# Performance work log

Hardware: AMD Instinct MI355X
Metric: run time of the kernel (lower is better)

Reference implementation:

```python
import jax, jax.numpy as jnp
import numpy as np

BN_EPS = 1e-5
ALPHA = 0.3
NEG = -9e9
BN_SCALE = 1.0 / np.sqrt(1.0 + BN_EPS)  # eval BatchNorm with running_mean=0, running_var=1


def gat_layer(x, mask, W, a, bn_g, bn_b, concat):
    # x: [B,N,Fin], mask: [B,N,N] bool, W: [Fin,Fo], a: [2*Fo]
    h = jnp.einsum('bnf,fo->bno', x, W)               # [B,N,Fo]
    Fo = W.shape[1]
    s1 = h @ a[:Fo]                                    # [B,N]
    s2 = h @ a[Fo:]                                    # [B,N]
    # additive decomposition of concat([h_i, h_j]) @ a (identical math)
    e = jax.nn.leaky_relu(s1[:, :, None] + s2[:, None, :], ALPHA)  # [B,N,N]
    att = jax.nn.softmax(jnp.where(mask, e, NEG), axis=-1)
    hp = jnp.einsum('bnm,bmo->bno', att, h)            # [B,N,Fo]
    # BatchNorm1d(nodes_num) in eval mode, per-node-channel affine
    hp = hp * BN_SCALE * bn_g[None, :, None] + bn_b[None, :, None]
    return jax.nn.elu(hp) if concat else hp


def setup_inputs() -> dict:
    key = jax.random.key(0)
    ks = jax.random.split(key, 10)
    B, N, F, Fo, H, C = 128, 200, 768, 32, 8, 2
    Fh = Fo * H
    return {
        'feat_matrix': jax.random.normal(ks[0], (B, N, F), jnp.float32),
        'adj': jax.random.randint(ks[1], (B, N, N), 0, 2, jnp.int32),
        'W_heads': jax.random.normal(ks[2], (H, F, Fo), jnp.float32) * 0.05,
        'a_heads': jax.random.normal(ks[3], (H, 2 * Fo), jnp.float32) * 0.1,
        'bnh_g': jnp.ones((H, N), jnp.float32),
        'bnh_b': jnp.zeros((H, N), jnp.float32),
        'bnt_g': jnp.ones((N,), jnp.float32),
        'bnt_b': jnp.zeros((N,), jnp.float32),
        'W_sent': jax.random.normal(ks[4], (Fh, C), jnp.float32) * 0.1,
        'a_sent': jax.random.normal(ks[5], (2 * C,), jnp.float32) * 0.1,
        'bns_g': jnp.ones((N,), jnp.float32),
        'bns_b': jnp.zeros((N,), jnp.float32),
        'W_para': jax.random.normal(ks[6], (Fh, C), jnp.float32) * 0.1,
        'a_para': jax.random.normal(ks[7], (2 * C,), jnp.float32) * 0.1,
        'bnp_g': jnp.ones((N,), jnp.float32),
        'bnp_b': jnp.zeros((N,), jnp.float32),
        'W_q': jax.random.normal(ks[8], (Fh, Fo), jnp.float32) * 0.1,
        'a_q': jax.random.normal(ks[9], (2 * Fo,), jnp.float32) * 0.1,
        'bnq_g': jnp.ones((N,), jnp.float32),
        'bnq_b': jnp.zeros((N,), jnp.float32),
        'W2': jax.random.normal(jax.random.fold_in(key, 99), (Fo, 2), jnp.float32) * 0.1,
    }


def reference(feat_matrix, adj, W_heads, a_heads, bnh_g, bnh_b, bnt_g, bnt_b,
              W_sent, a_sent, bns_g, bns_b, W_para, a_para, bnp_g, bnp_b,
              W_q, a_q, bnq_g, bnq_b, W2):
    mask = adj > 0
    # 8 attention heads (concat=True), vmapped over head dim
    heads = jax.vmap(lambda W, a, g, b: gat_layer(feat_matrix, mask, W, a, g, b, True))(
        W_heads, a_heads, bnh_g, bnh_b)              # [H,B,N,Fo]
    H, B, N, Fo = heads.shape
    x = jnp.moveaxis(heads, 0, 2).reshape(B, N, H * Fo)  # head-major concat, matches torch.cat
    # top-level BatchNorm1d (eval) + dropout(no-op)
    x = x * BN_SCALE * bnt_g[None, :, None] + bnt_b[None, :, None]
    logits_sent = jax.nn.sigmoid(gat_layer(x, mask, W_sent, a_sent, bns_g, bns_b, False))
    logits_para = jax.nn.elu(gat_layer(x, mask, W_para, a_para, bnp_g, bnp_b, False))
    q = gat_layer(x, mask, W_q, a_q, bnq_g, bnq_b, False)[:, 0, :]   # [B,Fo]
    logits_Qtype = jax.nn.elu(q @ W2).reshape(-1, 2)
    return (logits_sent, logits_para, logits_Qtype)
```

## Files before the change

kernel.cpp:

```cpp
#include <hip/hip_runtime.h>
#include <hip/hip_bf16.h>
#include <cstdint>

#define BN_SCALEF 0.99999500003749975f
#define EXP_SHIFT 4.0f


typedef _Float16 half8 __attribute__((ext_vector_type(8)));
typedef _Float16 half4 __attribute__((ext_vector_type(4)));
typedef float floatx4 __attribute__((ext_vector_type(4)));


__global__ __launch_bounds__(256) void prep(const int* __restrict__ adj,
                                            const float* __restrict__ W_heads,
                                            const float* __restrict__ Ws_in,
                                            const float* __restrict__ Wp_in,
                                            const float* __restrict__ Wq_in,
                                            const float* __restrict__ a_sent,
                                            const float* __restrict__ a_para,
                                            const float* __restrict__ a_q,
                                            unsigned int* __restrict__ maskw,
                                            _Float16* __restrict__ Bt,
                                            _Float16* __restrict__ W2t48) {
    int blk = blockIdx.x;
    int t = threadIdx.x;
    if (blk < 1600) {
        int w = t >> 6, lane = t & 63;
        for (int task = w; task < 64; task += 4) {
            int r = blk * 16 + (task >> 2);
            int c0 = (task & 3) * 64;
            int j = c0 + lane;
            bool v = (j < 200) && (adj[(size_t)r * 200 + j] > 0);
            unsigned long long m = __ballot(v ? 1 : 0);
            if (lane == 0) {
                maskw[r * 8 + (c0 >> 5)]     = (unsigned int)(m & 0xffffffffULL);
                maskw[r * 8 + (c0 >> 5) + 1] = (unsigned int)(m >> 32);
            }
        }
    } else if (blk < 1792) {
        __shared__ float ld[32][36];
        int blk2 = blk - 1600;
        int h = blk2 / 24, f0 = (blk2 % 24) * 32;
        int idx = t * 4;
        int fr = idx >> 5, o0 = idx & 31;
        float4 v = *(const float4*)&W_heads[(size_t)h * 24576 + (size_t)(f0 + fr) * 32 + o0];
        ld[fr][o0] = v.x; ld[fr][o0 + 1] = v.y; ld[fr][o0 + 2] = v.z; ld[fr][o0 + 3] = v.w;
        __syncthreads();
        int o = idx >> 5, fr0 = idx & 31;
        half4 hv;
#pragma unroll
        for (int u = 0; u < 4; ++u) hv[u] = (_Float16)ld[fr0 + u][o];
        *(half4*)&Bt[(size_t)(h * 32 + o) * 768 + f0 + fr0] = hv;
    } else {
        int k = t;
        for (int c = 0; c < 36; ++c) {
            float v;
            if (c < 2)      v = Ws_in[k * 2 + c];
            else if (c < 4) v = Wp_in[k * 2 + (c - 2)];
            else            v = Wq_in[k * 32 + (c - 4)];
            W2t48[c * 256 + k] = (_Float16)v;
        }
        W2t48[36 * 256 + k] = (_Float16)(Ws_in[k * 2] * a_sent[0] + Ws_in[k * 2 + 1] * a_sent[1]);
        W2t48[37 * 256 + k] = (_Float16)(Ws_in[k * 2] * a_sent[2] + Ws_in[k * 2 + 1] * a_sent[3]);
        W2t48[38 * 256 + k] = (_Float16)(Wp_in[k * 2] * a_para[0] + Wp_in[k * 2 + 1] * a_para[1]);
        W2t48[39 * 256 + k] = (_Float16)(Wp_in[k * 2] * a_para[2] + Wp_in[k * 2 + 1] * a_para[3]);
        float q1 = 0.f, q2 = 0.f;
#pragma unroll
        for (int o = 0; o < 32; ++o) {
            q1 += Wq_in[k * 32 + o] * a_q[o];
            q2 += Wq_in[k * 32 + o] * a_q[32 + o];
        }
        W2t48[40 * 256 + k] = (_Float16)q1;
        W2t48[41 * 256 + k] = (_Float16)q2;
        for (int c = 42; c < 48; ++c) W2t48[c * 256 + k] = (_Float16)0.f;
    }
}


__global__ __launch_bounds__(256) void gemm1_mfma(const float* __restrict__ A,
                                                  const _Float16* __restrict__ Bt,
                                                  _Float16* __restrict__ h16) {
    __shared__ __align__(16) _Float16 As[32 * 776];
    int t = threadIdx.x;
    int m0 = blockIdx.x * 32;

    {
        int row = t >> 3, kb = (t & 7) * 4;
        const float* ap = &A[(size_t)(m0 + row) * 768 + kb];
        _Float16* lp = &As[row * 776 + kb];
#pragma unroll
        for (int j = 0; j < 24; ++j) {
            float4 v = *(const float4*)(ap + j * 32);
            half4 hv;
            hv[0] = (_Float16)v.x; hv[1] = (_Float16)v.y;
            hv[2] = (_Float16)v.z; hv[3] = (_Float16)v.w;
            *(half4*)(lp + j * 32) = hv;
        }
    }
    __syncthreads();

    int w = t >> 6, lane = t & 63;
    int l16 = lane & 15, quad = lane >> 4;
    int c0 = w * 64;

    floatx4 acc[2][4];
#pragma unroll
    for (int i = 0; i < 2; ++i)
#pragma unroll
        for (int j = 0; j < 4; ++j) acc[i][j] = (floatx4){0.f, 0.f, 0.f, 0.f};

    const _Float16* bbase = &Bt[(size_t)(c0 + l16) * 768 + quad * 8];

    half8 nb[4];
#pragma unroll
    for (int ct = 0; ct < 4; ++ct)
        nb[ct] = *(const half8*)(bbase + (size_t)ct * 12288);

#pragma unroll 4
    for (int k0 = 0; k0 < 768; k0 += 32) {
        half8 bf0 = nb[0], bf1 = nb[1], bf2 = nb[2], bf3 = nb[3];
        int kn = (k0 + 32 < 768) ? (k0 + 32) : 0;
#pragma unroll
        for (int ct = 0; ct < 4; ++ct)
            nb[ct] = *(const half8*)(bbase + (size_t)ct * 12288 + kn);

        half8 af0 = *(half8*)&As[l16 * 776 + k0 + quad * 8];
        half8 af1 = *(half8*)&As[(16 + l16) * 776 + k0 + quad * 8];

        acc[0][0] = __builtin_amdgcn_mfma_f32_16x16x32_f16(af0, bf0, acc[0][0], 0, 0, 0);
        acc[1][0] = __builtin_amdgcn_mfma_f32_16x16x32_f16(af1, bf0, acc[1][0], 0, 0, 0);
        acc[0][1] = __builtin_amdgcn_mfma_f32_16x16x32_f16(af0, bf1, acc[0][1], 0, 0, 0);
        acc[1][1] = __builtin_amdgcn_mfma_f32_16x16x32_f16(af1, bf1, acc[1][1], 0, 0, 0);
        acc[0][2] = __builtin_amdgcn_mfma_f32_16x16x32_f16(af0, bf2, acc[0][2], 0, 0, 0);
        acc[1][2] = __builtin_amdgcn_mfma_f32_16x16x32_f16(af1, bf2, acc[1][2], 0, 0, 0);
        acc[0][3] = __builtin_amdgcn_mfma_f32_16x16x32_f16(af0, bf3, acc[0][3], 0, 0, 0);
        acc[1][3] = __builtin_amdgcn_mfma_f32_16x16x32_f16(af1, bf3, acc[1][3], 0, 0, 0);
    }

#pragma unroll
    for (int rt = 0; rt < 2; ++rt)
#pragma unroll
        for (int ct = 0; ct < 4; ++ct) {
            int gc = c0 + ct * 16 + l16;
#pragma unroll
            for (int r = 0; r < 4; ++r) {
                int gr = m0 + rt * 16 + quad * 4 + r;
                h16[(size_t)gr * 256 + gc] = (_Float16)acc[rt][ct][r];
            }
        }
}


__global__ __launch_bounds__(256) void attn_heads_mfma(
    const _Float16* __restrict__ h16,
    const float* __restrict__ a_h,
    const unsigned int* __restrict__ maskw,
    const float* __restrict__ bnh_g, const float* __restrict__ bnh_b,
    const float* __restrict__ bnt_g, const float* __restrict__ bnt_b,
    _Float16* __restrict__ x16h) {
    __shared__ __align__(16) _Float16 Bs[48 * 228];
    __shared__ __align__(16) _Float16 Ps[64 * 228];
    __shared__ float s1s[256], s2s[256];
    int hb = blockIdx.x;
    int h = hb >> 7, b = hb & 127;
    int t = threadIdx.x;

    unsigned long long* bz = (unsigned long long*)Bs;
    for (int idx = t; idx < (48 * 228) / 4; idx += 256) bz[idx] = 0ULL;
    __syncthreads();
    for (int idx = t; idx < 800; idx += 256) {
        int j = idx >> 2, w8 = (idx & 3) * 8;
        half8 v = *(const half8*)&h16[(size_t)(b * 200 + j) * 256 + h * 32 + w8];
#pragma unroll
        for (int u = 0; u < 8; ++u) Bs[(w8 + u) * 228 + j] = v[u];
    }
    if (t < 200) Bs[32 * 228 + t] = (_Float16)1.0f;
    __syncthreads();

    if (t < 200) {
        float acc1 = 0.f, acc2 = 0.f;
        const float* ab = &a_h[h * 64];
#pragma unroll
        for (int o = 0; o < 32; ++o) {
            float hv = (float)Bs[o * 228 + t];
            acc1 += hv * ab[o];
            acc2 += hv * ab[32 + o];
        }
        s1s[t] = acc1; s2s[t] = acc2;
    } else {
        s1s[t] = 0.f; s2s[t] = 0.f;
    }
    __syncthreads();

    int w = t >> 6, lane = t & 63;
    int l16 = lane & 15, quad = lane >> 4;
    _Float16* Pw = &Ps[w * 16 * 228];

    int j0 = lane * 4;
    float4 s2r = *(const float4*)&s2s[j0];
    const unsigned int* mbase = &maskw[(size_t)(b * 200) * 8 + (lane >> 3)];

    for (int tile = w; tile < 13; tile += 4) {
        int i_base = tile * 16;
        unsigned int mw = mbase[(size_t)i_base * 8];
        for (int r16 = 0; r16 < 16; ++r16) {
            int i = i_base + r16;
            unsigned int mw_next = 0;
            if (r16 < 15) {
                int in = i + 1; in = in < 200 ? in : 199;
                mw_next = mbase[(size_t)in * 8];
            }
            float s1v = s1s[i];
            half4 pv;
#pragma unroll
            for (int q = 0; q < 4; ++q) {
                float e = s1v + ((const float*)&s2r)[q];
                e = fmaxf(e, 0.3f * e);
                float p = ((mw >> ((j0 + q) & 31)) & 1u) ? __expf(e - EXP_SHIFT) : 0.f;
                pv[q] = (_Float16)p;
            }
            if (j0 < 228) *(half4*)&Pw[r16 * 228 + j0] = pv;
            mw = mw_next;
        }
        floatx4 acc0 = {0.f, 0.f, 0.f, 0.f};
        floatx4 acc1 = {0.f, 0.f, 0.f, 0.f};
        floatx4 acc2 = {0.f, 0.f, 0.f, 0.f};
#pragma unroll
        for (int kt = 0; kt < 7; ++kt) {
            half8 af = *(half8*)&Pw[l16 * 228 + kt * 32 + quad * 8];
            half8 b0 = *(half8*)&Bs[(l16) * 228 + kt * 32 + quad * 8];
            half8 b1 = *(half8*)&Bs[(16 + l16) * 228 + kt * 32 + quad * 8];
            half8 b2 = *(half8*)&Bs[(32 + l16) * 228 + kt * 32 + quad * 8];
            acc0 = __builtin_amdgcn_mfma_f32_16x16x32_f16(af, b0, acc0, 0, 0, 0);
            acc1 = __builtin_amdgcn_mfma_f32_16x16x32_f16(af, b1, acc1, 0, 0, 0);
            acc2 = __builtin_amdgcn_mfma_f32_16x16x32_f16(af, b2, acc2, 0, 0, 0);
        }
#pragma unroll
        for (int r = 0; r < 4; ++r) {
            int i = i_base + quad * 4 + r;
            float rsum = __shfl(acc2[r], (lane & 48), 64);
            if (i < 200) {
                float inv = 1.f / rsum;
                float g1 = BN_SCALEF * bnh_g[h * 200 + i], c1 = bnh_b[h * 200 + i];
                float g2 = BN_SCALEF * bnt_g[i], c2 = bnt_b[i];
                float v0 = acc0[r] * inv * g1 + c1;
                v0 = v0 > 0.f ? v0 : __expf(v0) - 1.f;
                v0 = v0 * g2 + c2;
                float v1 = acc1[r] * inv * g1 + c1;
                v1 = v1 > 0.f ? v1 : __expf(v1) - 1.f;
                v1 = v1 * g2 + c2;
                size_t base = (size_t)h * 819200 + (size_t)(b * 200 + i) * 32;
                x16h[base + l16]      = (_Float16)v0;
                x16h[base + 16 + l16] = (_Float16)v1;
            }
        }
    }
}


__global__ __launch_bounds__(256) void gemm2m(const _Float16* __restrict__ Xh,
                                              const _Float16* __restrict__ Wt,
                                              float* __restrict__ H2p) {
    __shared__ __align__(16) _Float16 Xs[64 * 264];
    __shared__ __align__(16) _Float16 Ws[48 * 264];
    int t = threadIdx.x;
    int m0 = blockIdx.x * 64;
    int srow = t >> 2, schunk = (t & 3) * 8;
#pragma unroll
    for (int h = 0; h < 8; ++h) {
        half8 v = *(const half8*)&Xh[(size_t)h * 819200 + (size_t)(m0 + srow) * 32 + schunk];
        *(half8*)&Xs[srow * 264 + h * 32 + schunk] = v;
    }
#pragma unroll
    for (int p = 0; p < 6; ++p) {
        int g = t + 256 * p;
        int n = g >> 5, ko = (g & 31) * 8;
        *(half8*)&Ws[n * 264 + ko] = *(const half8*)&Wt[(size_t)n * 256 + ko];
    }
    __syncthreads();

    int w = t >> 6, lane = t & 63;
    int l16 = lane & 15, quad = lane >> 4;
    int rbase = w * 16;
    floatx4 acc[3];
#pragma unroll
    for (int c = 0; c < 3; ++c) acc[c] = (floatx4){0.f, 0.f, 0.f, 0.f};
#pragma unroll
    for (int kt = 0; kt < 8; ++kt) {
        half8 af = *(half8*)&Xs[(rbase + l16) * 264 + kt * 32 + quad * 8];
#pragma unroll
        for (int ct = 0; ct < 3; ++ct) {
            half8 bf = *(half8*)&Ws[(ct * 16 + l16) * 264 + kt * 32 + quad * 8];
            acc[ct] = __builtin_amdgcn_mfma_f32_16x16x32_f16(af, bf, acc[ct], 0, 0, 0);
        }
    }
#pragma unroll
    for (int ct = 0; ct < 3; ++ct) {
        int col = ct * 16 + l16;
#pragma unroll
        for (int r = 0; r < 4; ++r) {
            int row = m0 + rbase + quad * 4 + r;
            H2p[(size_t)row * 48 + col] = acc[ct][r];
        }
    }
}


__global__ __launch_bounds__(256) void attn_spq(const float* __restrict__ H2p,
                                                const unsigned int* __restrict__ maskw,
                                                const float* __restrict__ bns_g, const float* __restrict__ bns_b,
                                                const float* __restrict__ bnp_g, const float* __restrict__ bnp_b,
                                                const float* __restrict__ bnq_g, const float* __restrict__ bnq_b,
                                                const float* __restrict__ W2, float* __restrict__ out) {
    int b = blockIdx.x;
    int t = threadIdx.x;
    if (blockIdx.y == 2) {
        __shared__ float p_lds[200];
        __shared__ float redd[4];
        __shared__ float red2[256];
        float s1v = H2p[(size_t)(b * 200) * 48 + 40];
        float p = 0.f;
        if (t < 200) {
            unsigned int mw = maskw[(size_t)(b * 200) * 8 + (t >> 5)];
            if ((mw >> (t & 31)) & 1u) {
                float x = s1v + H2p[(size_t)(b * 200 + t) * 48 + 41];
                x = fmaxf(x, 0.3f * x);
                p = __expf(x - EXP_SHIFT);
            }
            p_lds[t] = p;
        }
        float ds = p;
        for (int off = 32; off; off >>= 1) ds += __shfl_xor(ds, off, 64);
        if ((t & 63) == 0) redd[t >> 6] = ds;
        __syncthreads();
        ds = redd[0] + redd[1] + redd[2] + redd[3];
        int o = t & 31, g = t >> 5;
        float acc = 0.f;
        for (int j = g; j < 200; j += 8)
            acc += p_lds[j] * H2p[(size_t)(b * 200 + j) * 48 + 4 + o];
        red2[t] = acc;
        __syncthreads();
        if (t < 32) {
            float s = 0.f;
#pragma unroll
            for (int gg = 0; gg < 8; ++gg) s += red2[gg * 32 + t];
            float qv = (s / ds) * (BN_SCALEF * bnq_g[0]) + bnq_b[0];
            float c0 = qv * W2[t * 2], c1 = qv * W2[t * 2 + 1];
#pragma unroll
            for (int off = 16; off; off >>= 1) {
                c0 += __shfl_xor(c0, off, 64);
                c1 += __shfl_xor(c1, off, 64);
            }
            if (t == 0) {
                out[102400 + b * 2 + 0] = c0 > 0.f ? c0 : __expf(c0) - 1.f;
                out[102400 + b * 2 + 1] = c1 > 0.f ? c1 : __expf(c1) - 1.f;
            }
        }
        return;
    }
    __shared__ float s2s[200], s2p[200];
    __shared__ float s1sA[200], s1pA[200];
    __shared__ __align__(16) float hsp[200 * 4];
    int chunk = blockIdx.y;
    if (t < 200) {
        const float* hr = &H2p[(size_t)(b * 200 + t) * 48];
        float4 hv = *(const float4*)hr;
        *(float4*)&hsp[t * 4] = hv;
        s1sA[t] = hr[36]; s2s[t] = hr[37];
        s1pA[t] = hr[38]; s2p[t] = hr[39];
    }
    __syncthreads();
    int w = t >> 6, lane = t & 63;
    for (int it = 0; it < 25; ++it) {
        int i = chunk * 100 + it * 4 + w;
        float s1sv = s1sA[i];
        float s1pv = s1pA[i];
        float ds = 0.f, dp = 0.f, pa0 = 0.f, pa1 = 0.f, pb0 = 0.f, pb1 = 0.f;
#pragma unroll
        for (int q = 0; q < 4; ++q) {
            int j = lane + 64 * q;
            if (j < 200) {
                unsigned int mw = maskw[(size_t)(b * 200 + i) * 8 + (j >> 5)];
                if ((mw >> (j & 31)) & 1u) {
                    float x1 = s1sv + s2s[j]; x1 = fmaxf(x1, 0.3f * x1);
                    float x2 = s1pv + s2p[j]; x2 = fmaxf(x2, 0.3f * x2);
                    float p1 = __expf(x1 - EXP_SHIFT), p2 = __expf(x2 - EXP_SHIFT);
                    ds += p1; dp += p2;
                    float4 hv = *(float4*)&hsp[j * 4];
                    pa0 += p1 * hv.x; pa1 += p1 * hv.y;
                    pb0 += p2 * hv.z; pb1 += p2 * hv.w;
                }
            }
        }
        for (int off = 32; off; off >>= 1) {
            ds  += __shfl_xor(ds, off, 64);  dp  += __shfl_xor(dp, off, 64);
            pa0 += __shfl_xor(pa0, off, 64); pa1 += __shfl_xor(pa1, off, 64);
            pb0 += __shfl_xor(pb0, off, 64); pb1 += __shfl_xor(pb1, off, 64);
        }
        if (lane == 0) {
            float gs = BN_SCALEF * bns_g[i], bs = bns_b[i];
            float v0 = (pa0 / ds) * gs + bs, v1 = (pa1 / ds) * gs + bs;
            out[(size_t)(b * 200 + i) * 2 + 0] = 1.f / (1.f + __expf(-v0));
            out[(size_t)(b * 200 + i) * 2 + 1] = 1.f / (1.f + __expf(-v1));
            float gp = BN_SCALEF * bnp_g[i], bp = bnp_b[i];
            float u0 = (pb0 / dp) * gp + bp, u1 = (pb1 / dp) * gp + bp;
            out[51200 + (size_t)(b * 200 + i) * 2 + 0] = u0 > 0.f ? u0 : __expf(u0) - 1.f;
            out[51200 + (size_t)(b * 200 + i) * 2 + 1] = u1 > 0.f ? u1 : __expf(u1) - 1.f;
        }
    }
}


extern "C" void kernel_launch(void* const* d_in, const int* in_sizes, int n_in,
                              void* d_out, int out_size, void* d_ws, size_t ws_size,
                              hipStream_t stream) {
    (void)in_sizes; (void)n_in; (void)out_size; (void)ws_size;
    const float* feat    = (const float*)d_in[0];
    const int*   adj     = (const int*)d_in[1];
    const float* W_heads = (const float*)d_in[2];
    const float* a_heads = (const float*)d_in[3];
    const float* bnh_g   = (const float*)d_in[4];
    const float* bnh_b   = (const float*)d_in[5];
    const float* bnt_g   = (const float*)d_in[6];
    const float* bnt_b   = (const float*)d_in[7];
    const float* W_sent  = (const float*)d_in[8];
    const float* a_sent  = (const float*)d_in[9];
    const float* bns_g   = (const float*)d_in[10];
    const float* bns_b   = (const float*)d_in[11];
    const float* W_para  = (const float*)d_in[12];
    const float* a_para  = (const float*)d_in[13];
    const float* bnp_g   = (const float*)d_in[14];
    const float* bnp_b   = (const float*)d_in[15];
    const float* W_q     = (const float*)d_in[16];
    const float* a_q     = (const float*)d_in[17];
    const float* bnq_g   = (const float*)d_in[18];
    const float* bnq_b   = (const float*)d_in[19];
    const float* W2      = (const float*)d_in[20];
    float* out = (float*)d_out;
    float* ws  = (float*)d_ws;

    _Float16* h16   = (_Float16*)ws;
    _Float16* x16h  = (_Float16*)(ws + 3276800);
    _Float16* W2t48 = (_Float16*)(ws + 6553600);
    _Float16* Bt    = (_Float16*)(ws + 6559744);
    unsigned int* maskw = (unsigned int*)(ws + 6658048);
    float* H2p   = ws + 6862848;

    prep<<<dim3(1793), dim3(256), 0, stream>>>(adj, W_heads, W_sent, W_para, W_q,
                                               a_sent, a_para, a_q, maskw, Bt, W2t48);
    gemm1_mfma<<<dim3(800), dim3(256), 0, stream>>>(feat, Bt, h16);
    attn_heads_mfma<<<dim3(1024), dim3(256), 0, stream>>>(h16, a_heads, maskw,
                                                          bnh_g, bnh_b, bnt_g, bnt_b, x16h);
    gemm2m<<<dim3(400), dim3(256), 0, stream>>>(x16h, W2t48, H2p);
    attn_spq<<<dim3(128, 3), dim3(256), 0, stream>>>(H2p, maskw, bns_g, bns_b,
                                                     bnp_g, bnp_b, bnq_g, bnq_b, W2, out);
}
```

Baseline: 296.4 us.

## Pipeline gemm1 A tiles via async global-to-LDS loads with 64-row blocks

Rewrites the first projection GEMM so that fp32 A tiles stream into a 4-stage LDS ring using global_load_lds direct copies, with an XOR swizzle. Each K-step is fenced by a waitcnt and a barrier, so loading overlaps the MFMA work instead of staging the whole 32x768 row block before compute. Blocks grow to 64 rows and 512 threads, so each B fragment is reused by two row-waves. The fp16 conversion now happens at fragment-read time from fp32 LDS. The risks are a per-step barrier cost and hand-tuned vmcnt counts that must match the number of outstanding loads.

```diff
diff --git a/kernel.cpp b/kernel.cpp
--- a/kernel.cpp
+++ b/kernel.cpp
@@ -77,55 +77,78 @@
 }
 
 
-__global__ __launch_bounds__(256) void gemm1_mfma(const float* __restrict__ A,
+typedef __attribute__((address_space(1))) const unsigned int* gp1_t;
+typedef __attribute__((address_space(3))) unsigned int* lp3_t;
+#define GLOAD16(g, l) __builtin_amdgcn_global_load_lds((gp1_t)(g), (lp3_t)(l), 16, 0, 0)
+
+__global__ __launch_bounds__(512) void gemm1_mfma(const float* __restrict__ A,
                                                   const _Float16* __restrict__ Bt,
                                                   _Float16* __restrict__ h16) {
-    __shared__ __align__(16) _Float16 As[32 * 776];
+    __shared__ __align__(16) float As[4][64 * 32];
     int t = threadIdx.x;
-    int m0 = blockIdx.x * 32;
-
-    {
-        int row = t >> 3, kb = (t & 7) * 4;
-        const float* ap = &A[(size_t)(m0 + row) * 768 + kb];
-        _Float16* lp = &As[row * 776 + kb];
-#pragma unroll
-        for (int j = 0; j < 24; ++j) {
-            float4 v = *(const float4*)(ap + j * 32);
-            half4 hv;
-            hv[0] = (_Float16)v.x; hv[1] = (_Float16)v.y;
-            hv[2] = (_Float16)v.z; hv[3] = (_Float16)v.w;
-            *(half4*)(lp + j * 32) = hv;
-        }
-    }
-    __syncthreads();
+    int m0 = blockIdx.x * 64;
 
     int w = t >> 6, lane = t & 63;
-    int l16 = lane & 15, quad = lane >> 4;
-    int c0 = w * 64;
-
-    floatx4 acc[2][4];
-#pragma unroll
-    for (int i = 0; i < 2; ++i)
-#pragma unroll
-        for (int j = 0; j < 4; ++j) acc[i][j] = (floatx4){0.f, 0.f, 0.f, 0.f};
+    int wr = w >> 2, wc = w & 3;
+    int quad = lane >> 4, l16 = lane & 15;
+    int c0 = wc * 64;
+
+    int sr = t >> 3, sp = t & 7;
+    int sj = sp ^ (sr & 7);
+    const float* agbase = &A[(size_t)(m0 + sr) * 768 + sj * 4];
+    float* ldsw[4];
+#pragma unroll
+    for (int s = 0; s < 4; ++s) ldsw[s] = &As[s][w * 256];
+
+#define STAGE(s, kt) GLOAD16(agbase + (kt) * 32, ldsw[s])
 
     const _Float16* bbase = &Bt[(size_t)(c0 + l16) * 768 + quad * 8];
 
+    STAGE(0, 0);
     half8 nb[4];
 #pragma unroll
     for (int ct = 0; ct < 4; ++ct)
         nb[ct] = *(const half8*)(bbase + (size_t)ct * 12288);
-
-#pragma unroll 4
-    for (int k0 = 0; k0 < 768; k0 += 32) {
+    STAGE(1, 1);
+
+    floatx4 acc[2][4];
+#pragma unroll
+    for (int i = 0; i < 2; ++i)
+#pragma unroll
+        for (int j = 0; j < 4; ++j) acc[i][j] = (floatx4){0.f, 0.f, 0.f, 0.f};
+
+    asm volatile("s_waitcnt vmcnt(5)" ::: "memory");
+    __builtin_amdgcn_s_barrier();
+    __builtin_amdgcn_sched_barrier(0);
+
+    int p0 = (2 * quad) ^ (l16 & 7);
+    const int rowA0 = (wr * 32 + l16) * 32;
+    const int rowA1 = (wr * 32 + 16 + l16) * 32;
+
+    for (int k = 0; k < 24; ++k) {
+        int kbn = (k + 1 < 24 ? k + 1 : 23) * 32;
         half8 bf0 = nb[0], bf1 = nb[1], bf2 = nb[2], bf3 = nb[3];
-        int kn = (k0 + 32 < 768) ? (k0 + 32) : 0;
 #pragma unroll
         for (int ct = 0; ct < 4; ++ct)
-            nb[ct] = *(const half8*)(bbase + (size_t)ct * 12288 + kn);
-
-        half8 af0 = *(half8*)&As[l16 * 776 + k0 + quad * 8];
-        half8 af1 = *(half8*)&As[(16 + l16) * 776 + k0 + quad * 8];
+            nb[ct] = *(const half8*)(bbase + (size_t)ct * 12288 + kbn);
+
+        int kst = (k + 2 < 24) ? (k + 2) : 23;
+        STAGE((k + 2) & 3, kst);
+
+        const float* ab = As[k & 3];
+        float4 x00 = *(const float4*)(ab + rowA0 + p0 * 4);
+        float4 x01 = *(const float4*)(ab + rowA0 + (p0 ^ 1) * 4);
+        float4 x10 = *(const float4*)(ab + rowA1 + p0 * 4);
+        float4 x11 = *(const float4*)(ab + rowA1 + (p0 ^ 1) * 4);
+        half8 af0, af1;
+        af0[0] = (_Float16)x00.x; af0[1] = (_Float16)x00.y;
+        af0[2] = (_Float16)x00.z; af0[3] = (_Float16)x00.w;
+        af0[4] = (_Float16)x01.x; af0[5] = (_Float16)x01.y;
+        af0[6] = (_Float16)x01.z; af0[7] = (_Float16)x01.w;
+        af1[0] = (_Float16)x10.x; af1[1] = (_Float16)x10.y;
+        af1[2] = (_Float16)x10.z; af1[3] = (_Float16)x10.w;
+        af1[4] = (_Float16)x11.x; af1[5] = (_Float16)x11.y;
+        af1[6] = (_Float16)x11.z; af1[7] = (_Float16)x11.w;
 
         acc[0][0] = __builtin_amdgcn_mfma_f32_16x16x32_f16(af0, bf0, acc[0][0], 0, 0, 0);
         acc[1][0] = __builtin_amdgcn_mfma_f32_16x16x32_f16(af1, bf0, acc[1][0], 0, 0, 0);
@@ -135,8 +158,13 @@
         acc[1][2] = __builtin_amdgcn_mfma_f32_16x16x32_f16(af1, bf2, acc[1][2], 0, 0, 0);
         acc[0][3] = __builtin_amdgcn_mfma_f32_16x16x32_f16(af0, bf3, acc[0][3], 0, 0, 0);
         acc[1][3] = __builtin_amdgcn_mfma_f32_16x16x32_f16(af1, bf3, acc[1][3], 0, 0, 0);
-    }
-
+
+        asm volatile("s_waitcnt vmcnt(5)" ::: "memory");
+        __builtin_amdgcn_s_barrier();
+        __builtin_amdgcn_sched_barrier(0);
+    }
+
+    int rbase = m0 + wr * 32;
 #pragma unroll
     for (int rt = 0; rt < 2; ++rt)
 #pragma unroll
@@ -144,10 +172,11 @@
             int gc = c0 + ct * 16 + l16;
 #pragma unroll
             for (int r = 0; r < 4; ++r) {
-                int gr = m0 + rt * 16 + quad * 4 + r;
+                int gr = rbase + rt * 16 + quad * 4 + r;
                 h16[(size_t)gr * 256 + gc] = (_Float16)acc[rt][ct][r];
             }
         }
+#undef STAGE
 }
 
 
@@ -448,7 +477,7 @@
 
     prep<<<dim3(1793), dim3(256), 0, stream>>>(adj, W_heads, W_sent, W_para, W_q,
                                                a_sent, a_para, a_q, maskw, Bt, W2t48);
-    gemm1_mfma<<<dim3(800), dim3(256), 0, stream>>>(feat, Bt, h16);
+    gemm1_mfma<<<dim3(400), dim3(512), 0, stream>>>(feat, Bt, h16);
     attn_heads_mfma<<<dim3(1024), dim3(256), 0, stream>>>(h16, a_heads, maskw,
                                                           bnh_g, bnh_b, bnt_g, bnt_b, x16h);
     gemm2m<<<dim3(400), dim3(256), 0, stream>>>(x16h, W2t48, H2p);
```

Result: no change. 299.6 us (+1.1%).
